# Optimization experiments

Measured on AMD Instinct MI355X. Metric: run time of the kernel, lower is better.

## Reference

```python
import jax, jax.numpy as jnp
import numpy as np

B, NQ, NKV = 2, 1024, 4096
DQ = 1024          # query_dim == context_dim
H, DH = 16, 64     # heads, dim_head
INNER = H * DH     # 1024
SCALE = DH ** -0.5


def setup_inputs() -> dict:
    key = jax.random.key(0)
    ks = jax.random.split(key, 6)
    s = 1.0 / np.sqrt(DQ)
    return {
        "x": jax.random.normal(ks[0], (B, NQ, DQ), dtype=jnp.float32),
        "context": jax.random.normal(ks[1], (B, NKV, DQ), dtype=jnp.float32),
        "Wq": jax.random.normal(ks[2], (DQ, INNER), dtype=jnp.float32) * s,
        "Wkv": jax.random.normal(ks[3], (DQ, 2 * INNER), dtype=jnp.float32) * s,
        "Wout": jax.random.normal(ks[4], (INNER, DQ), dtype=jnp.float32) * (1.0 / np.sqrt(INNER)),
        "b_out": jax.random.normal(ks[5], (DQ,), dtype=jnp.float32) * 0.01,
    }


def _split_heads(t):
    # b n (h d) -> b h n d
    b, n, _ = t.shape
    return t.reshape(b, n, H, DH).transpose(0, 2, 1, 3)


def reference(x, context, Wq, Wkv, Wout, b_out):
    q = x @ Wq                       # [B, NQ, INNER]
    kv = context @ Wkv               # [B, NKV, 2*INNER]
    k, v = jnp.split(kv, 2, axis=-1)
    q, k, v = map(_split_heads, (q, k, v))          # [B, H, n, DH]
    sim = jnp.einsum("bhid,bhjd->bhij", q, k) * SCALE  # [B, H, NQ, NKV]
    attn = jax.nn.softmax(sim, axis=-1)
    out = jnp.einsum("bhij,bhjd->bhid", attn, v)       # [B, H, NQ, DH]
    out = out.transpose(0, 2, 1, 3).reshape(B, NQ, INNER)  # (b h) n d -> b n (h d)
    return out @ Wout + b_out
```

## Files before the change

### kernel.cpp

```cpp
#include <hip/hip_runtime.h>
#include <stdint.h>

#define B_    2
#define NQ_   1024
#define NKV_  4096
#define DQ_   1024
#define H_    16
#define DH_   64
#define INNER_ 1024

typedef unsigned short u16;
typedef uint32_t u32;
typedef __bf16 bf16x8 __attribute__((ext_vector_type(8)));
typedef float  f32x4  __attribute__((ext_vector_type(4)));

__device__ __forceinline__ u16 f2bf(float x) {
  union { float f; uint32_t u; } v; v.f = x;
  uint32_t r = v.u + 0x7FFFu + ((v.u >> 16) & 1u);
  return (u16)(r >> 16);
}
__device__ __forceinline__ u32 pack2(float a, float b) {
  return (u32)f2bf(a) | ((u32)f2bf(b) << 16);
}
__device__ __forceinline__ u32 pack2rn(float a, float b) {
  union { float f; u32 u; } x, y; x.f = a; y.f = b;
  return __builtin_amdgcn_perm(y.u + 0x8000u, x.u + 0x8000u, 0x07060302u);
}
__device__ __forceinline__ float bf2f(u16 s) {
  union { float f; uint32_t u; } v; v.u = ((uint32_t)s) << 16; return v.f;
}

__device__ __forceinline__ void gload16(const void* g, void* l) {
  __builtin_amdgcn_global_load_lds((const __attribute__((address_space(1))) void*)g,
                                   (__attribute__((address_space(3))) void*)l,
                                   16, 0, 0);
}

__global__ __launch_bounds__(256) void prep(const float* __restrict__ x,
                                            const float* __restrict__ ctx,
                                            const float* __restrict__ Wq,
                                            const float* __restrict__ Wkv,
                                            const float* __restrict__ Wout,
                                            u16* __restrict__ xb,
                                            u16* __restrict__ ctxb,
                                            u16* __restrict__ WqT,
                                            u16* __restrict__ WkvT,
                                            u16* __restrict__ WoutT) {
  int bid = blockIdx.x;
  if (bid < 10240) {
    const float* src; u16* dst; int blk;
    if (bid < 2048) { src = x; dst = xb; blk = bid; }
    else            { src = ctx; dst = ctxb; blk = bid - 2048; }
    int i = (blk * 256 + threadIdx.x) * 4;
    float4 v = *(const float4*)(src + i);
    uint2 o; o.x = pack2(v.x, v.y); o.y = pack2(v.z, v.w);
    *(uint2*)(dst + i) = o;
    return;
  }
  __shared__ float tile[32][33];
  const float* W; u16* Wt; int K, N, local, nsh;
  if (bid < 11264)      { W = Wq;   Wt = WqT;   K = 1024; N = 1024; local = bid - 10240; nsh = 5; }
  else if (bid < 13312) { W = Wkv;  Wt = WkvT;  K = 1024; N = 2048; local = bid - 11264; nsh = 6; }
  else                  { W = Wout; Wt = WoutT; K = 1024; N = 1024; local = bid - 13312; nsh = 5; }
  int n0 = (local & ((1 << nsh) - 1)) * 32;
  int k0 = (local >> nsh) * 32;
  int tx = threadIdx.x & 31, ty = threadIdx.x >> 5;
  for (int i = ty; i < 32; i += 8)
    tile[i][tx] = W[(size_t)(k0 + i) * N + n0 + tx];
  __syncthreads();
  for (int i = ty; i < 32; i += 8)
    Wt[(size_t)(n0 + i) * K + k0 + tx] = f2bf(tile[tx][i]);
}

__global__ __launch_bounds__(512, 2) void kv_gemm(const u16* __restrict__ ctxb,
                                                  const u16* __restrict__ WkvT,
                                                  u16* __restrict__ kb,
                                                  u16* __restrict__ vTb) {
  __shared__ __align__(16) u16 As[2][256 * 64];
  __shared__ __align__(16) u16 Bs[2][256 * 64];
  const int tid = threadIdx.x;
  const int lane = tid & 63;
  const int w = tid >> 6;
  const int wr = w >> 2, wc = w & 3;
  const int l15 = lane & 15, quad = lane >> 4;
  const int K = 1024;

  int bid = blockIdx.x;
  int wgid = (bid & 7) * 32 + (bid >> 3);
  const int tm = wgid >> 3, tn = wgid & 7;
  const int m0 = tm * 256, n0 = tn * 256;
  const u16* Ag = ctxb + (size_t)m0 * K;
  const u16* Bg = WkvT + (size_t)n0 * K;

  size_t offA[2][2], offB[2][2];
#pragma unroll
  for (int ah = 0; ah < 2; ++ah)
#pragma unroll
    for (int p = 0; p < 2; ++p) {
      int c = p * 512 + (w << 6) + lane;
      int s = ah * 128 + (c >> 3);
      int col = ((c & 7) ^ (s & 7)) << 3;
      int rA = ((s >> 6) & 1) * 128 + ((s >> 7) & 1) * 64 + (s & 63);
      int rB = ((s >> 5) & 3) * 64 + ((s >> 7) & 1) * 32 + (s & 31);
      offA[ah][p] = (size_t)rA * 1024 + col;
      offB[ah][p] = (size_t)rB * 1024 + col;
    }

#define STAGE_A(bufi, ah, kk) do { \
    gload16(Ag + offA[ah][0] + (kk), &As[bufi][(ah) * 8192 + (w << 9)]); \
    gload16(Ag + offA[ah][1] + (kk), &As[bufi][(ah) * 8192 + 4096 + (w << 9)]); \
  } while (0)
#define STAGE_B(bufi, bh, kk) do { \
    gload16(Bg + offB[bh][0] + (kk), &Bs[bufi][(bh) * 8192 + (w << 9)]); \
    gload16(Bg + offB[bh][1] + (kk), &Bs[bufi][(bh) * 8192 + 4096 + (w << 9)]); \
  } while (0)
#define LDA2(dst, i8, bufi) do { \
    const int _s = ((i8) >> 2) * 128 + wr * 64 + ((i8) & 3) * 16 + l15; \
    const u16* _p = &As[bufi][_s * 64]; const int _x = _s & 7; \
    dst[0] = *(const bf16x8*)&_p[(quad ^ _x) << 3]; \
    dst[1] = *(const bf16x8*)&_p[((quad + 4) ^ _x) << 3]; \
  } while (0)
#define LDB2(dst, j, bufi) do { \
    const int _s = ((j) >> 1) * 128 + wc * 32 + ((j) & 1) * 16 + l15; \
    const u16* _p = &Bs[bufi][_s * 64]; const int _x = _s & 7; \
    dst[0] = *(const bf16x8*)&_p[(quad ^ _x) << 3]; \
    dst[1] = *(const bf16x8*)&_p[((quad + 4) ^ _x) << 3]; \
  } while (0)
#define MF(i0, j0, bb) do { \
    _Pragma("unroll") \
    for (int _i = 0; _i < 4; ++_i) { \
      acc[(i0) + _i][(j0)    ] = __builtin_amdgcn_mfma_f32_16x16x32_bf16(a[_i][0], bb[0][0], acc[(i0) + _i][(j0)    ], 0, 0, 0); \
      acc[(i0) + _i][(j0)    ] = __builtin_amdgcn_mfma_f32_16x16x32_bf16(a[_i][1], bb[0][1], acc[(i0) + _i][(j0)    ], 0, 0, 0); \
      acc[(i0) + _i][(j0) + 1] = __builtin_amdgcn_mfma_f32_16x16x32_bf16(a[_i][0], bb[1][0], acc[(i0) + _i][(j0) + 1], 0, 0, 0); \
      acc[(i0) + _i][(j0) + 1] = __builtin_amdgcn_mfma_f32_16x16x32_bf16(a[_i][1], bb[1][1], acc[(i0) + _i][(j0) + 1], 0, 0, 0); \
    } \
  } while (0)

  f32x4 acc[8][4] = {};
  bf16x8 a[4][2], b[2][2], c2[2][2];

  STAGE_A(0, 0, 0);
  STAGE_B(0, 0, 0);
  STAGE_B(0, 1, 0);
  STAGE_A(0, 1, 0);
  asm volatile("s_waitcnt vmcnt(4)" ::: "memory");
  __builtin_amdgcn_s_barrier();

#define KTILE(cur, nxt, kk, STG, W1, W2) do { \
     \
    LDB2(b[0], 0, cur); LDB2(b[1], 1, cur); \
    LDA2(a[0], 0, cur); LDA2(a[1], 1, cur); LDA2(a[2], 2, cur); LDA2(a[3], 3, cur); \
    if (STG) STAGE_A(nxt, 0, kk); \
    __builtin_amdgcn_s_barrier(); \
    asm volatile("s_waitcnt lgkmcnt(0)" ::: "memory"); \
    __builtin_amdgcn_s_setprio(1); MF(0, 0, b); __builtin_amdgcn_s_setprio(0); \
    asm volatile("s_waitcnt " W1 ::: "memory"); \
    __builtin_amdgcn_s_barrier(); \
     \
    LDB2(c2[0], 2, cur); LDB2(c2[1], 3, cur); \
    if (STG) STAGE_B(nxt, 0, kk); \
    __builtin_amdgcn_s_barrier(); \
    asm volatile("s_waitcnt lgkmcnt(0)" ::: "memory"); \
    __builtin_amdgcn_s_setprio(1); MF(0, 2, c2); __builtin_amdgcn_s_setprio(0); \
    asm volatile("s_waitcnt " W2 ::: "memory"); \
    __builtin_amdgcn_s_barrier(); \
     \
    LDA2(a[0], 4, cur); LDA2(a[1], 5, cur); LDA2(a[2], 6, cur); LDA2(a[3], 7, cur); \
    if (STG) STAGE_B(nxt, 1, kk); \
    __builtin_amdgcn_s_barrier(); \
    asm volatile("s_waitcnt lgkmcnt(0)" ::: "memory"); \
    __builtin_amdgcn_s_setprio(1); MF(4, 0, b); __builtin_amdgcn_s_setprio(0); \
    __builtin_amdgcn_s_barrier(); \
     \
    if (STG) STAGE_A(nxt, 1, kk); \
    __builtin_amdgcn_s_barrier(); \
    __builtin_amdgcn_s_setprio(1); MF(4, 2, c2); __builtin_amdgcn_s_setprio(0); \
    if (STG) { asm volatile("s_waitcnt vmcnt(4)" ::: "memory"); } \
    __builtin_amdgcn_s_barrier(); \
  } while (0)

  for (int T = 0; T < 15; ++T) {
    const int cur = T & 1, nxt = cur ^ 1, kk = (T + 1) * 64;
    KTILE(cur, nxt, kk, 1, "vmcnt(4)", "vmcnt(4)");
  }
  KTILE(1, 0, 0, 0, "vmcnt(2)", "vmcnt(0)");

  if (tn < 4) {
#pragma unroll
    for (int i8 = 0; i8 < 8; ++i8)
#pragma unroll
      for (int j = 0; j < 4; ++j) {
        int col = n0 + wc * 64 + j * 16 + l15;
#pragma unroll
        for (int r = 0; r < 4; ++r) {
          int row = m0 + wr * 128 + i8 * 16 + quad * 4 + r;
          kb[(size_t)row * 1024 + col] = f2bf(acc[i8][j][r]);
        }
      }
  } else {
    const int bb_ = m0 >> 12;
#pragma unroll
    for (int i8 = 0; i8 < 8; ++i8) {
      int kvr = (m0 & 4095) + wr * 128 + i8 * 16 + quad * 4;
#pragma unroll
      for (int j = 0; j < 4; ++j) {
        int c = (n0 - 1024) + wc * 64 + j * 16 + l15;
        int h = c >> 6, dh = c & 63;
        uint2 st;
        st.x = pack2(acc[i8][j][0], acc[i8][j][1]);
        st.y = pack2(acc[i8][j][2], acc[i8][j][3]);
        *(uint2*)&vTb[((size_t)((bb_ * 16 + h) * 64 + dh)) * NKV_ + kvr] = st;
      }
    }
  }
#undef STAGE_A
#undef STAGE_B
#undef LDA2
#undef LDB2
#undef MF
#undef KTILE
}

__global__ __launch_bounds__(256) void q_gemm(const u16* __restrict__ A,
                                              const u16* __restrict__ Bt,
                                              u16* __restrict__ outp) {
  __shared__ __align__(16) u16 As[64 * 32];
  __shared__ __align__(16) u16 Bs[128 * 32];
  const int tid = threadIdx.x;
  const int lane = tid & 63;
  const int w = tid >> 6;
  const int wr = w >> 1, wc = w & 1;
  const int l15 = lane & 15, quad = lane >> 4;
  const int unit = blockIdx.x;
  const int m0 = (unit >> 3) * 64, n0 = (unit & 7) * 128;
  const int K = 1024, N = 1024;

  const u16* Ab = A + (size_t)m0 * K;
  const u16* Bb = Bt + (size_t)n0 * K;
  f32x4 acc[2][4] = {};

  const int ar = tid >> 2, ac = (tid & 3) << 3;
  const int q1 = w * 64 + lane, q2 = q1 + 256;
  const int br1 = q1 >> 2, bc1 = (q1 & 3) << 3;
  const int br2 = q2 >> 2, bc2 = (q2 & 3) << 3;

  for (int k0 = 0; k0 < K; k0 += 32) {
    __syncthreads();
    gload16(Ab + (size_t)ar * K + k0 + ac, &As[w * 512]);
    gload16(Bb + (size_t)br1 * K + k0 + bc1, &Bs[w * 512]);
    gload16(Bb + (size_t)br2 * K + k0 + bc2, &Bs[2048 + w * 512]);
    __syncthreads();
    bf16x8 af[2], bfr[4];
#pragma unroll
    for (int i = 0; i < 2; ++i)
      af[i] = *(const bf16x8*)&As[(wr * 32 + i * 16 + l15) * 32 + quad * 8];
#pragma unroll
    for (int j = 0; j < 4; ++j)
      bfr[j] = *(const bf16x8*)&Bs[(wc * 64 + j * 16 + l15) * 32 + quad * 8];
#pragma unroll
    for (int i = 0; i < 2; ++i)
#pragma unroll
      for (int j = 0; j < 4; ++j)
        acc[i][j] = __builtin_amdgcn_mfma_f32_16x16x32_bf16(af[i], bfr[j], acc[i][j], 0, 0, 0);
  }

#pragma unroll
  for (int i = 0; i < 2; ++i)
#pragma unroll
    for (int j = 0; j < 4; ++j) {
      int col = n0 + wc * 64 + j * 16 + l15;
#pragma unroll
      for (int r = 0; r < 4; ++r) {
        int row = m0 + wr * 32 + i * 16 + quad * 4 + r;
        outp[(size_t)row * N + col] = f2bf(acc[i][j][r]);
      }
    }
}

__global__ __launch_bounds__(256) void out_gemm(const u16* __restrict__ A,
                                                const u16* __restrict__ Bt,
                                                float* __restrict__ Cout,
                                                const float* __restrict__ bias) {
  __shared__ __align__(16) u16 As[64 * 32];
  __shared__ __align__(16) u16 Bs[128 * 32];
  const int tid = threadIdx.x;
  const int lane = tid & 63;
  const int w = tid >> 6;
  const int wr = w >> 1, wc = w & 1;
  const int l15 = lane & 15, quad = lane >> 4;
  const int unit = blockIdx.x;
  const int m0 = (unit >> 3) * 64, n0 = (unit & 7) * 128;
  const int K = 1024, N = 1024;

  const u16* Ab = A + (size_t)m0 * K;
  const u16* Bb = Bt + (size_t)n0 * K;
  f32x4 acc[2][4] = {};

  const int ar = tid >> 2, ac = (tid & 3) << 3;
  const int q1 = w * 64 + lane, q2 = q1 + 256;
  const int br1 = q1 >> 2, bc1 = (q1 & 3) << 3;
  const int br2 = q2 >> 2, bc2 = (q2 & 3) << 3;

  for (int k0 = 0; k0 < K; k0 += 32) {
    __syncthreads();
    gload16(Ab + (size_t)ar * K + k0 + ac, &As[w * 512]);
    gload16(Bb + (size_t)br1 * K + k0 + bc1, &Bs[w * 512]);
    gload16(Bb + (size_t)br2 * K + k0 + bc2, &Bs[2048 + w * 512]);
    __syncthreads();
    bf16x8 af[2], bfr[4];
#pragma unroll
    for (int i = 0; i < 2; ++i)
      af[i] = *(const bf16x8*)&As[(wr * 32 + i * 16 + l15) * 32 + quad * 8];
#pragma unroll
    for (int j = 0; j < 4; ++j)
      bfr[j] = *(const bf16x8*)&Bs[(wc * 64 + j * 16 + l15) * 32 + quad * 8];
#pragma unroll
    for (int i = 0; i < 2; ++i)
#pragma unroll
      for (int j = 0; j < 4; ++j)
        acc[i][j] = __builtin_amdgcn_mfma_f32_16x16x32_bf16(af[i], bfr[j], acc[i][j], 0, 0, 0);
  }

#pragma unroll
  for (int i = 0; i < 2; ++i)
#pragma unroll
    for (int j = 0; j < 4; ++j) {
      int col = n0 + wc * 64 + j * 16 + l15;
      float bv = bias[col];
#pragma unroll
      for (int r = 0; r < 4; ++r) {
        int row = m0 + wr * 32 + i * 16 + quad * 4 + r;
        Cout[(size_t)row * N + col] = acc[i][j][r] + bv;
      }
    }
}

__global__ __launch_bounds__(256, 2) void attn_kernel(const u16* __restrict__ qg,
                                                      const u16* __restrict__ kb,
                                                      const u16* __restrict__ vT,
                                                      u16* __restrict__ attn_out) {
  __shared__ __align__(16) u16 Ks[128 * 64];
  __shared__ __align__(16) u16 Vs[64 * 128];
  __shared__ __align__(16) u32 P32[4 * 4 * 16 * 20];
  __shared__ float Lr[4][4][16];

  const int tid = threadIdx.x;
  const int lane = tid & 63;
  const int w = tid >> 6;
  const int l15 = lane & 15, quad = lane >> 4;
  const int bh = blockIdx.x, b = bh >> 4, h = bh & 15;
  const int q0 = blockIdx.y * 64;

  const float SC = 0.125f * 1.44269504088896340736f;
  union { u16 s[8]; bf16x8 v; } qf[4][2];
#pragma unroll
  for (int t = 0; t < 4; ++t)
#pragma unroll
    for (int kc = 0; kc < 2; ++kc) {
      const u16* qp = qg + (size_t)(b * NQ_ + q0 + t * 16 + l15) * INNER_ + h * 64 +
                      kc * 32 + quad * 8;
      union { u16 s[8]; uint4 u; } tmp;
      tmp.u = *(const uint4*)qp;
#pragma unroll
      for (int e = 0; e < 8; ++e) qf[t][kc].s[e] = f2bf(bf2f(tmp.s[e]) * SC);
    }

  f32x4 Oacc[4][4] = {};
  float l_lane[4] = {0.f, 0.f, 0.f, 0.f};

  for (int it = 0; it < 32; ++it) {
    const int j0 = it * 128;
    __syncthreads();
#pragma unroll
    for (int i = 0; i < 4; ++i) {
      int s = i * 256 + tid;
      int kr = s >> 3, kg = (s ^ kr) & 7;
      gload16(kb + (size_t)(b * NKV_ + j0 + kr) * 1024 + h * 64 + kg * 8,
              &Ks[(i * 256 + w * 64) * 8]);
      int vr = s >> 4, vg = (s ^ vr) & 15;
      gload16(vT + (size_t)(bh * 64 + vr) * NKV_ + j0 + vg * 8,
              &Vs[(i * 256 + w * 64) * 8]);
    }
    __syncthreads();

    bf16x8 kf[2][2];
#pragma unroll
    for (int kvt = 0; kvt < 2; ++kvt)
#pragma unroll
      for (int kc = 0; kc < 2; ++kc)
        kf[kvt][kc] = *(const bf16x8*)
          &Ks[(w * 32 + kvt * 16 + l15) * 64 + (((kc * 4 + quad) ^ l15) & 7) * 8];
    f32x4 sacc[2][4] = {};
#pragma unroll
    for (int kvt = 0; kvt < 2; ++kvt)
#pragma unroll
      for (int t = 0; t < 4; ++t)
#pragma unroll
        for (int kc = 0; kc < 2; ++kc)
          sacc[kvt][t] = __builtin_amdgcn_mfma_f32_16x16x32_bf16(
              kf[kvt][kc], qf[t][kc].v, sacc[kvt][t], 0, 0, 0);

#pragma unroll
    for (int kvt = 0; kvt < 2; ++kvt)
#pragma unroll
      for (int t = 0; t < 4; ++t) {
        float p0 = __builtin_amdgcn_exp2f(sacc[kvt][t][0]);
        float p1 = __builtin_amdgcn_exp2f(sacc[kvt][t][1]);
        float p2 = __builtin_amdgcn_exp2f(sacc[kvt][t][2]);
        float p3 = __builtin_amdgcn_exp2f(sacc[kvt][t][3]);
        l_lane[t] += (p0 + p1) + (p2 + p3);
        uint2 pk; pk.x = pack2rn(p0, p1); pk.y = pack2rn(p2, p3);
        *(uint2*)&P32[((w * 4 + t) * 16 + l15) * 20 + kvt * 8 + quad * 2] = pk;
      }

    bf16x8 vf[4], pf[4];
#pragma unroll
    for (int d = 0; d < 4; ++d)
      vf[d] = *(const bf16x8*)
        &Vs[(d * 16 + l15) * 128 + (((w * 4 + quad) ^ l15) & 15) * 8];
#pragma unroll
    for (int t = 0; t < 4; ++t)
      pf[t] = *(const bf16x8*)&P32[((w * 4 + t) * 16 + l15) * 20 + quad * 4];
#pragma unroll
    for (int d = 0; d < 4; ++d)
#pragma unroll
      for (int t = 0; t < 4; ++t)
        Oacc[d][t] = __builtin_amdgcn_mfma_f32_16x16x32_bf16(vf[d], pf[t], Oacc[d][t],
                                                             0, 0, 0);
  }

#pragma unroll
  for (int t = 0; t < 4; ++t) {
    l_lane[t] += __shfl_xor(l_lane[t], 16);
    l_lane[t] += __shfl_xor(l_lane[t], 32);
  }
  if (quad == 0) {
#pragma unroll
    for (int t = 0; t < 4; ++t) Lr[w][t][l15] = l_lane[t];
  }
  __syncthreads();
  float inv = 1.0f / (Lr[0][w][l15] + Lr[1][w][l15] + Lr[2][w][l15] + Lr[3][w][l15]);

  float* red = (float*)P32;
  u16* ob = attn_out + (size_t)(b * NQ_ + q0 + w * 16 + l15) * INNER_ + h * 64;
#pragma unroll
  for (int d = 0; d < 4; ++d) {
    __syncthreads();
#pragma unroll
    for (int t = 0; t < 4; ++t)
      *(f32x4*)&red[(w * 4 + t) * 256 + quad * 64 + l15 * 4] = Oacc[d][t];
    __syncthreads();
    f32x4 r = *(const f32x4*)&red[(0 * 4 + w) * 256 + quad * 64 + l15 * 4];
#pragma unroll
    for (int ww = 1; ww < 4; ++ww) {
      f32x4 c = *(const f32x4*)&red[(ww * 4 + w) * 256 + quad * 64 + l15 * 4];
      r[0] += c[0]; r[1] += c[1]; r[2] += c[2]; r[3] += c[3];
    }
    *(u32*)(ob + d * 16 + quad * 4)     = pack2(r[0] * inv, r[1] * inv);
    *(u32*)(ob + d * 16 + quad * 4 + 2) = pack2(r[2] * inv, r[3] * inv);
  }
}

extern "C" void kernel_launch(void* const* d_in, const int* in_sizes, int n_in,
                              void* d_out, int out_size, void* d_ws, size_t ws_size,
                              hipStream_t stream) {
  const float* x    = (const float*)d_in[0];
  const float* ctx  = (const float*)d_in[1];
  const float* Wq   = (const float*)d_in[2];
  const float* Wkv  = (const float*)d_in[3];
  const float* Wout = (const float*)d_in[4];
  const float* bout = (const float*)d_in[5];

  char* ws = (char*)d_ws;
  u16* xb    = (u16*)(ws + (size_t)( 0u << 20));
  u16* ab    = (u16*)(ws + (size_t)( 0u << 20));
  u16* ctxb  = (u16*)(ws + (size_t)( 4u << 20));
  u16* WqT   = (u16*)(ws + (size_t)(20u << 20));
  u16* WkvT  = (u16*)(ws + (size_t)(22u << 20));
  u16* WoutT = (u16*)(ws + (size_t)(26u << 20));
  u16* qb    = (u16*)(ws + (size_t)(28u << 20));
  u16* kb    = (u16*)(ws + (size_t)(32u << 20));
  u16* vTb   = (u16*)(ws + (size_t)(48u << 20));

  prep<<<14336, 256, 0, stream>>>(x, ctx, Wq, Wkv, Wout, xb, ctxb, WqT, WkvT, WoutT);
  q_gemm<<<256, 256, 0, stream>>>(xb, WqT, qb);
  kv_gemm<<<256, 512, 0, stream>>>(ctxb, WkvT, kb, vTb);
  attn_kernel<<<dim3(32, 16), 256, 0, stream>>>(qb, kb, vTb, ab);
  out_gemm<<<256, 256, 0, stream>>>(ab, WoutT, (float*)d_out, bout);
}
```

Before: 228.3 us.

## Load K and V fragments directly from global memory, dropping LDS staging

The attention kernel no longer stages K and V tiles in shared memory behind two block barriers per iteration. Each wave now reads its own K rows and transposed-V fragments straight from global memory into registers, and occupancy is raised to 3 blocks per SM because LDS use drops. The aim is to remove barrier stalls and LDS traffic. The cost is uncoalesced 16-byte global loads with no cross-wave reuse, so the kernel leans on L2/cache and on exposed load latency, since nothing is prefetched.

```diff
diff --git a/kernel.cpp b/kernel.cpp
--- a/kernel.cpp
+++ b/kernel.cpp
@@ -335,12 +335,10 @@
     }
 }
 
-__global__ __launch_bounds__(256, 2) void attn_kernel(const u16* __restrict__ qg,
+__global__ __launch_bounds__(256, 3) void attn_kernel(const u16* __restrict__ qg,
                                                       const u16* __restrict__ kb,
                                                       const u16* __restrict__ vT,
                                                       u16* __restrict__ attn_out) {
-  __shared__ __align__(16) u16 Ks[128 * 64];
-  __shared__ __align__(16) u16 Vs[64 * 128];
   __shared__ __align__(16) u32 P32[4 * 4 * 16 * 20];
   __shared__ float Lr[4][4][16];
 
@@ -365,59 +363,44 @@
       for (int e = 0; e < 8; ++e) qf[t][kc].s[e] = f2bf(bf2f(tmp.s[e]) * SC);
     }
 
+  const u16* kb_l = kb + ((size_t)(b * NKV_) + l15) * 1024 + h * 64 + quad * 8;
+  const u16* vT_l = vT + ((size_t)(bh * 64) + l15) * NKV_ + quad * 8;
+
   f32x4 Oacc[4][4] = {};
   float l_lane[4] = {0.f, 0.f, 0.f, 0.f};
 
   for (int it = 0; it < 32; ++it) {
-    const int j0 = it * 128;
-    __syncthreads();
-#pragma unroll
-    for (int i = 0; i < 4; ++i) {
-      int s = i * 256 + tid;
-      int kr = s >> 3, kg = (s ^ kr) & 7;
-      gload16(kb + (size_t)(b * NKV_ + j0 + kr) * 1024 + h * 64 + kg * 8,
-              &Ks[(i * 256 + w * 64) * 8]);
-      int vr = s >> 4, vg = (s ^ vr) & 15;
-      gload16(vT + (size_t)(bh * 64 + vr) * NKV_ + j0 + vg * 8,
-              &Vs[(i * 256 + w * 64) * 8]);
-    }
-    __syncthreads();
-
-    bf16x8 kf[2][2];
-#pragma unroll
-    for (int kvt = 0; kvt < 2; ++kvt)
-#pragma unroll
-      for (int kc = 0; kc < 2; ++kc)
-        kf[kvt][kc] = *(const bf16x8*)
-          &Ks[(w * 32 + kvt * 16 + l15) * 64 + (((kc * 4 + quad) ^ l15) & 7) * 8];
-    f32x4 sacc[2][4] = {};
-#pragma unroll
-    for (int kvt = 0; kvt < 2; ++kvt)
-#pragma unroll
-      for (int t = 0; t < 4; ++t)
-#pragma unroll
-        for (int kc = 0; kc < 2; ++kc)
-          sacc[kvt][t] = __builtin_amdgcn_mfma_f32_16x16x32_bf16(
-              kf[kvt][kc], qf[t][kc].v, sacc[kvt][t], 0, 0, 0);
-
-#pragma unroll
-    for (int kvt = 0; kvt < 2; ++kvt)
+    const int jw = it * 128 + w * 32;
+
+    bf16x8 vf[4];
+#pragma unroll
+    for (int d = 0; d < 4; ++d)
+      vf[d] = *(const bf16x8*)(vT_l + (size_t)(d * 16) * NKV_ + jw);
+
+#pragma unroll
+    for (int kvt = 0; kvt < 2; ++kvt) {
+      const u16* krow = kb_l + (size_t)(jw + kvt * 16) * 1024;
+      bf16x8 k0 = *(const bf16x8*)(krow);
+      bf16x8 k1 = *(const bf16x8*)(krow + 32);
+      f32x4 sacc[4] = {};
 #pragma unroll
       for (int t = 0; t < 4; ++t) {
-        float p0 = __builtin_amdgcn_exp2f(sacc[kvt][t][0]);
-        float p1 = __builtin_amdgcn_exp2f(sacc[kvt][t][1]);
-        float p2 = __builtin_amdgcn_exp2f(sacc[kvt][t][2]);
-        float p3 = __builtin_amdgcn_exp2f(sacc[kvt][t][3]);
+        sacc[t] = __builtin_amdgcn_mfma_f32_16x16x32_bf16(k0, qf[t][0].v, sacc[t], 0, 0, 0);
+        sacc[t] = __builtin_amdgcn_mfma_f32_16x16x32_bf16(k1, qf[t][1].v, sacc[t], 0, 0, 0);
+      }
+#pragma unroll
+      for (int t = 0; t < 4; ++t) {
+        float p0 = __builtin_amdgcn_exp2f(sacc[t][0]);
+        float p1 = __builtin_amdgcn_exp2f(sacc[t][1]);
+        float p2 = __builtin_amdgcn_exp2f(sacc[t][2]);
+        float p3 = __builtin_amdgcn_exp2f(sacc[t][3]);
         l_lane[t] += (p0 + p1) + (p2 + p3);
         uint2 pk; pk.x = pack2rn(p0, p1); pk.y = pack2rn(p2, p3);
         *(uint2*)&P32[((w * 4 + t) * 16 + l15) * 20 + kvt * 8 + quad * 2] = pk;
       }
-
-    bf16x8 vf[4], pf[4];
-#pragma unroll
-    for (int d = 0; d < 4; ++d)
-      vf[d] = *(const bf16x8*)
-        &Vs[(d * 16 + l15) * 128 + (((w * 4 + quad) ^ l15) & 15) * 8];
+    }
+
+    bf16x8 pf[4];
 #pragma unroll
     for (int t = 0; t < 4; ++t)
       pf[t] = *(const bf16x8*)&P32[((w * 4 + t) * 16 + l15) * 20 + quad * 4];
```

Result: slower. 270.9 us (+18.7%).

## Prefetch next KV tile during attention compute and coarsen prep conversion blocks

Applied to the files above, without the earlier changes.

The attention loop now issues the global-to-LDS loads for the next K/V tile right after the current tile's K and V fragments are read into registers. This lets those loads overlap the QK MFMA, softmax and PV MFMA work instead of stalling at the top of each iteration. It also raises wave priority around the MFMA blocks. Separately, the prep kernel's fp32-to-bf16 conversion now does 8 float4s per thread, which cuts the launch to fewer blocks. The risk is that it still uses a single LDS buffer, so correctness depends on every wave having read its fragments before the barrier. V registers also stay live longer, which raises register pressure.

```diff
diff --git a/kernel.cpp b/kernel.cpp
--- a/kernel.cpp
+++ b/kernel.cpp
@@ -47,21 +47,25 @@
                                             u16* __restrict__ WkvT,
                                             u16* __restrict__ WoutT) {
   int bid = blockIdx.x;
-  if (bid < 10240) {
-    const float* src; u16* dst; int blk;
-    if (bid < 2048) { src = x; dst = xb; blk = bid; }
-    else            { src = ctx; dst = ctxb; blk = bid - 2048; }
-    int i = (blk * 256 + threadIdx.x) * 4;
-    float4 v = *(const float4*)(src + i);
-    uint2 o; o.x = pack2(v.x, v.y); o.y = pack2(v.z, v.w);
-    *(uint2*)(dst + i) = o;
+  if (bid < 1280) {
+    const float* src; u16* dst; int fbase;
+    if (bid < 256) { src = x;   dst = xb;   fbase = bid * 2048; }
+    else           { src = ctx; dst = ctxb; fbase = (bid - 256) * 2048; }
+#pragma unroll
+    for (int u = 0; u < 8; ++u) {
+      int i = (fbase + u * 256 + threadIdx.x) * 4;
+      float4 v = *(const float4*)(src + i);
+      uint2 o; o.x = pack2(v.x, v.y); o.y = pack2(v.z, v.w);
+      *(uint2*)(dst + i) = o;
+    }
     return;
   }
   __shared__ float tile[32][33];
   const float* W; u16* Wt; int K, N, local, nsh;
-  if (bid < 11264)      { W = Wq;   Wt = WqT;   K = 1024; N = 1024; local = bid - 10240; nsh = 5; }
-  else if (bid < 13312) { W = Wkv;  Wt = WkvT;  K = 1024; N = 2048; local = bid - 11264; nsh = 6; }
-  else                  { W = Wout; Wt = WoutT; K = 1024; N = 1024; local = bid - 13312; nsh = 5; }
+  int b2 = bid - 1280;
+  if (b2 < 1024)      { W = Wq;   Wt = WqT;   K = 1024; N = 1024; local = b2;        nsh = 5; }
+  else if (b2 < 3072) { W = Wkv;  Wt = WkvT;  K = 1024; N = 2048; local = b2 - 1024; nsh = 6; }
+  else                { W = Wout; Wt = WoutT; K = 1024; N = 1024; local = b2 - 3072; nsh = 5; }
   int n0 = (local & ((1 << nsh) - 1)) * 32;
   int k0 = (local >> nsh) * 32;
   int tx = threadIdx.x & 31, ty = threadIdx.x >> 5;
@@ -365,22 +369,25 @@
       for (int e = 0; e < 8; ++e) qf[t][kc].s[e] = f2bf(bf2f(tmp.s[e]) * SC);
     }
 
+#define STAGEKV(j0) do { \
+    _Pragma("unroll") \
+    for (int i_ = 0; i_ < 4; ++i_) { \
+      int s_ = i_ * 256 + tid; \
+      int kr = s_ >> 3, kg = (s_ ^ kr) & 7; \
+      gload16(kb + (size_t)(b * NKV_ + (j0) + kr) * 1024 + h * 64 + kg * 8, \
+              &Ks[(i_ * 256 + w * 64) * 8]); \
+      int vr = s_ >> 4, vg = (s_ ^ vr) & 15; \
+      gload16(vT + (size_t)(bh * 64 + vr) * NKV_ + (j0) + vg * 8, \
+              &Vs[(i_ * 256 + w * 64) * 8]); \
+    } \
+  } while (0)
+
   f32x4 Oacc[4][4] = {};
   float l_lane[4] = {0.f, 0.f, 0.f, 0.f};
 
+  STAGEKV(0);
+
   for (int it = 0; it < 32; ++it) {
-    const int j0 = it * 128;
-    __syncthreads();
-#pragma unroll
-    for (int i = 0; i < 4; ++i) {
-      int s = i * 256 + tid;
-      int kr = s >> 3, kg = (s ^ kr) & 7;
-      gload16(kb + (size_t)(b * NKV_ + j0 + kr) * 1024 + h * 64 + kg * 8,
-              &Ks[(i * 256 + w * 64) * 8]);
-      int vr = s >> 4, vg = (s ^ vr) & 15;
-      gload16(vT + (size_t)(bh * 64 + vr) * NKV_ + j0 + vg * 8,
-              &Vs[(i * 256 + w * 64) * 8]);
-    }
     __syncthreads();
 
     bf16x8 kf[2][2];
@@ -390,7 +397,18 @@
       for (int kc = 0; kc < 2; ++kc)
         kf[kvt][kc] = *(const bf16x8*)
           &Ks[(w * 32 + kvt * 16 + l15) * 64 + (((kc * 4 + quad) ^ l15) & 7) * 8];
+    bf16x8 vf[4];
+#pragma unroll
+    for (int d = 0; d < 4; ++d)
+      vf[d] = *(const bf16x8*)
+        &Vs[(d * 16 + l15) * 128 + (((w * 4 + quad) ^ l15) & 15) * 8];
+
+    __syncthreads();
+
+    if (it < 31) STAGEKV((it + 1) * 128);
+
     f32x4 sacc[2][4] = {};
+    __builtin_amdgcn_s_setprio(1);
 #pragma unroll
     for (int kvt = 0; kvt < 2; ++kvt)
 #pragma unroll
@@ -399,6 +417,7 @@
         for (int kc = 0; kc < 2; ++kc)
           sacc[kvt][t] = __builtin_amdgcn_mfma_f32_16x16x32_bf16(
               kf[kvt][kc], qf[t][kc].v, sacc[kvt][t], 0, 0, 0);
+    __builtin_amdgcn_s_setprio(0);
 
 #pragma unroll
     for (int kvt = 0; kvt < 2; ++kvt)
@@ -413,21 +432,20 @@
         *(uint2*)&P32[((w * 4 + t) * 16 + l15) * 20 + kvt * 8 + quad * 2] = pk;
       }
 
-    bf16x8 vf[4], pf[4];
-#pragma unroll
-    for (int d = 0; d < 4; ++d)
-      vf[d] = *(const bf16x8*)
-        &Vs[(d * 16 + l15) * 128 + (((w * 4 + quad) ^ l15) & 15) * 8];
+    bf16x8 pf[4];
 #pragma unroll
     for (int t = 0; t < 4; ++t)
       pf[t] = *(const bf16x8*)&P32[((w * 4 + t) * 16 + l15) * 20 + quad * 4];
+    __builtin_amdgcn_s_setprio(1);
 #pragma unroll
     for (int d = 0; d < 4; ++d)
 #pragma unroll
       for (int t = 0; t < 4; ++t)
         Oacc[d][t] = __builtin_amdgcn_mfma_f32_16x16x32_bf16(vf[d], pf[t], Oacc[d][t],
                                                              0, 0, 0);
-  }
+    __builtin_amdgcn_s_setprio(0);
+  }
+#undef STAGEKV
 
 #pragma unroll
   for (int t = 0; t < 4; ++t) {
@@ -482,7 +500,7 @@
   u16* kb    = (u16*)(ws + (size_t)(32u << 20));
   u16* vTb   = (u16*)(ws + (size_t)(48u << 20));
 
-  prep<<<14336, 256, 0, stream>>>(x, ctx, Wq, Wkv, Wout, xb, ctxb, WqT, WkvT, WoutT);
+  prep<<<5376, 256, 0, stream>>>(x, ctx, Wq, Wkv, Wout, xb, ctxb, WqT, WkvT, WoutT);
   q_gemm<<<256, 256, 0, stream>>>(xb, WqT, qb);
   kv_gemm<<<256, 512, 0, stream>>>(ctxb, WkvT, kb, vTb);
   attn_kernel<<<dim3(32, 16), 256, 0, stream>>>(qb, kb, vTb, ab);
```

Measured after the change: 228.5 us. Within noise of the previous version (+0.1%).
